# Kernel tuning notes

Measured on AMD Instinct MI355X. Metric: run time of the kernel, lower is better.

## Reference

```python
import jax, jax.numpy as jnp
import numpy as np

GRID = 5          # grid_size
DEG = 3           # spline_degree
NC = GRID + DEG   # num_coeffs = 8
IN = 4            # input_dim
HID = 4           # hidden_dim
N = 524288        # batch
TAU = 1.0         # gumbel_tau


def get_knots(knot_deltas):
    # softplus deltas normalized to span [-1, 1], then clamp-pad ends DEG times
    d = jax.nn.softplus(knot_deltas)
    dn = d / d.sum() * 2.0
    interior = -1.0 + jnp.cumsum(dn)                      # [GRID+1]
    knots = jnp.concatenate([jnp.array([-1.0], dtype=d.dtype), interior[:-1],
                             jnp.array([1.0], dtype=d.dtype)])  # [GRID+2]
    pad0 = jnp.full((DEG,), knots[0], dtype=d.dtype)
    pad1 = jnp.full((DEG,), knots[-1], dtype=d.dtype)
    return jnp.concatenate([pad0, knots, pad1])           # [GRID+2+2*DEG]


def b_spline_basis(x, knots):
    # x: [N]; Cox-de Boor recursion, degree-0 -> DEG
    xe = x[:, None]
    basis = ((xe >= knots[:-1]) & (xe < knots[1:])).astype(x.dtype)
    basis = basis.at[:, -1].add((x == knots[-1]).astype(x.dtype))
    for d in range(1, DEG + 1):
        b1, b2 = basis[:, :-1], basis[:, 1:]
        n = b1.shape[1]
        ki, kid = knots[:n], knots[d:d + n]
        ki1, kid1 = knots[1:1 + n], knots[d + 1:d + 1 + n]
        den1, den2 = kid - ki, kid1 - ki1
        m1, m2 = den1 > 1e-8, den2 > 1e-8
        t1 = jnp.where(m1, (xe - ki) / jnp.where(m1, den1, 1.0) * b1, 0.0)
        t2 = jnp.where(m2, (kid1 - xe) / jnp.where(m2, den2, 1.0) * b2, 0.0)
        basis = t1 + t2
    return basis  # [N, GRID+1+DEG] = [N, NC+1]


def spline_apply(x, coeffs, knot_deltas):
    knots = get_knots(knot_deltas)
    b = b_spline_basis(x, knots)
    if b.shape[1] > NC:
        b = b[:, :NC]
    elif b.shape[1] < NC:
        b = jnp.pad(b, ((0, 0), (0, NC - b.shape[1])))
    return b @ coeffs  # [N]


spline_v = jax.vmap(spline_apply, in_axes=(0, 0, 0))  # over edges


def setup_inputs() -> dict:
    key = jax.random.key(0)
    ks = jax.random.split(key, 8)
    x = jax.random.uniform(ks[0], (N, IN), dtype=jnp.float32, minval=-1.0, maxval=1.0)
    l1_coeffs = jax.random.normal(ks[1], (HID * IN, NC), dtype=jnp.float32)
    l1_knot_deltas = jax.random.normal(ks[2], (HID * IN, GRID + 1), dtype=jnp.float32)
    op_alpha = jax.random.normal(ks[3], (HID, 2), dtype=jnp.float32)
    u = jax.random.uniform(ks[4], (HID, 2), dtype=jnp.float32, minval=1e-6, maxval=1.0 - 1e-6)
    gumbel_noise = -jnp.log(-jnp.log(u))
    l2_coeffs = jax.random.normal(ks[5], (HID, NC), dtype=jnp.float32)
    l2_knot_deltas = jax.random.normal(ks[6], (HID, GRID + 1), dtype=jnp.float32)
    base_offset = jax.random.normal(ks[7], (1,), dtype=jnp.float32)
    return {"x": x, "l1_coeffs": l1_coeffs, "l1_knot_deltas": l1_knot_deltas,
            "op_alpha": op_alpha, "gumbel_noise": gumbel_noise,
            "l2_coeffs": l2_coeffs, "l2_knot_deltas": l2_knot_deltas,
            "base_offset": base_offset}


def reference(x, l1_coeffs, l1_knot_deltas, op_alpha, gumbel_noise,
              l2_coeffs, l2_knot_deltas, base_offset):
    xT = x.T                                              # [IN, N]
    x_edges = jnp.broadcast_to(xT[None], (HID, IN, xT.shape[1])).reshape(HID * IN, -1)
    l1 = spline_v(x_edges, l1_coeffs, l1_knot_deltas).reshape(HID, IN, -1)
    sum_v = l1.sum(axis=1)                                # [HID, N]
    prod_v = jnp.clip(l1, -5.0, 5.0).prod(axis=1)         # [HID, N]
    w = jax.nn.softmax((op_alpha + gumbel_noise) / TAU, axis=-1)  # gumbel-softmax (soft)
    hidden = w[:, 0:1] * sum_v + w[:, 1:2] * prod_v       # [HID, N]
    l2 = spline_v(hidden, l2_coeffs, l2_knot_deltas)      # [HID, N]
    return l2.sum(axis=0)[:, None] + base_offset          # [N, 1]
```

## Files before the change

### kernel.cpp

```cpp
#include <hip/hip_runtime.h>
#include <math.h>

#define GRIDK   5
#define DEG     3
#define NC      8
#define IN_DIM  4
#define HID     4
#define NKNOT   13
#define NSPL    20
#define NPTS    524288

struct SplineTabs {
    float knots[NSPL][NKNOT];
    float inv1[NSPL][12];
    float inv2[NSPL][11];
    float inv3[NSPL][10];
    float coef[NSPL][9];
    float w0[HID];
    float w1[HID];
    float base;
};

__device__ __forceinline__ float softplusf(float x) {
    return fmaxf(x, 0.0f) + log1pf(expf(-fabsf(x)));
}

__device__ __forceinline__ float spline_eval(const SplineTabs& T, int s, float x) {
    bool in_dom = (x >= -1.0f) && (x < 1.0f);
    if (!in_dom) return 0.0f;

    const float* t = T.knots[s];
    int j = 3;
    j += (x >= t[4]);
    j += (x >= t[5]);
    j += (x >= t[6]);
    j += (x >= t[7]);
    j += (x >= t[8]);

    float l1v = x - t[j];
    float l2v = x - t[j - 1];
    float l3v = x - t[j - 2];
    float r1 = t[j + 1] - x;
    float r2 = t[j + 2] - x;
    float r3 = t[j + 3] - x;

    float temp, saved;
    temp = T.inv1[s][j];
    float N0 = r1 * temp;
    float N1 = l1v * temp;
    temp = N0 * T.inv2[s][j - 1];
    N0 = r1 * temp;
    saved = l2v * temp;
    temp = N1 * T.inv2[s][j];
    N1 = saved + r2 * temp;
    float N2 = l1v * temp;
    temp = N0 * T.inv3[s][j - 2];
    N0 = r1 * temp;
    saved = l3v * temp;
    temp = N1 * T.inv3[s][j - 1];
    N1 = saved + r2 * temp;
    saved = l2v * temp;
    temp = N2 * T.inv3[s][j];
    N2 = saved + r3 * temp;
    float N3 = l1v * temp;

    const float* c = T.coef[s];
    return N0 * c[j - 3] + N1 * c[j - 2] + N2 * c[j - 1] + N3 * c[j];
}

__global__ __launch_bounds__(256) void unified_kan_kernel(
    const float* __restrict__ x,
    const float* __restrict__ l1_coeffs,
    const float* __restrict__ l1_kd,
    const float* __restrict__ op_alpha,
    const float* __restrict__ gumbel,
    const float* __restrict__ l2_coeffs,
    const float* __restrict__ l2_kd,
    const float* __restrict__ base_offset,
    float* __restrict__ out)
{
    __shared__ SplineTabs T;
    const int tid = threadIdx.x;

    if (tid < NSPL) {
        const int s = tid;
        const float* deltas;
        const float* cf;
        if (s < HID * IN_DIM) { deltas = l1_kd + s * (GRIDK + 1); cf = l1_coeffs + s * NC; }
        else                  { deltas = l2_kd + (s - HID * IN_DIM) * (GRIDK + 1);
                                cf = l2_coeffs + (s - HID * IN_DIM) * NC; }

        float d[GRIDK + 1];
        float dsum = 0.0f;
        #pragma unroll
        for (int j = 0; j < GRIDK + 1; ++j) { d[j] = softplusf(deltas[j]); dsum += d[j]; }
        float scale = 2.0f / dsum;

        float t[NKNOT];
        t[0] = t[1] = t[2] = t[3] = -1.0f;
        float acc = 0.0f;
        #pragma unroll
        for (int j = 0; j < GRIDK; ++j) { acc += d[j] * scale; t[4 + j] = -1.0f + acc; }
        t[9] = t[10] = t[11] = t[12] = 1.0f;

        #pragma unroll
        for (int i = 0; i < NKNOT; ++i) T.knots[s][i] = t[i];
        #pragma unroll
        for (int i = 0; i < 12; ++i) { float den = t[i + 1] - t[i]; T.inv1[s][i] = (den > 1e-8f) ? 1.0f / den : 0.0f; }
        #pragma unroll
        for (int i = 0; i < 11; ++i) { float den = t[i + 2] - t[i]; T.inv2[s][i] = (den > 1e-8f) ? 1.0f / den : 0.0f; }
        #pragma unroll
        for (int i = 0; i < 10; ++i) { float den = t[i + 3] - t[i]; T.inv3[s][i] = (den > 1e-8f) ? 1.0f / den : 0.0f; }
        #pragma unroll
        for (int i = 0; i < NC; ++i) T.coef[s][i] = cf[i];
        T.coef[s][8] = 0.0f;
    } else if (tid < NSPL + HID) {
        const int h = tid - NSPL;
        float a0 = op_alpha[h * 2 + 0] + gumbel[h * 2 + 0];
        float a1 = op_alpha[h * 2 + 1] + gumbel[h * 2 + 1];
        float m = fmaxf(a0, a1);
        float e0 = expf(a0 - m), e1 = expf(a1 - m);
        float inv = 1.0f / (e0 + e1);
        T.w0[h] = e0 * inv;
        T.w1[h] = e1 * inv;
    } else if (tid == NSPL + HID) {
        T.base = base_offset[0];
    }
    __syncthreads();

    const int stride = gridDim.x * blockDim.x;
    for (int i = blockIdx.x * blockDim.x + tid; i < NPTS; i += stride) {
        float4 xv = reinterpret_cast<const float4*>(x)[i];
        float xin[IN_DIM] = {xv.x, xv.y, xv.z, xv.w};

        float acc = T.base;
        #pragma unroll
        for (int h = 0; h < HID; ++h) {
            float sum = 0.0f, prod = 1.0f;
            #pragma unroll
            for (int k = 0; k < IN_DIM; ++k) {
                float v = spline_eval(T, h * IN_DIM + k, xin[k]);
                sum += v;
                prod *= fminf(fmaxf(v, -5.0f), 5.0f);
            }
            float hid = T.w0[h] * sum + T.w1[h] * prod;
            acc += spline_eval(T, HID * IN_DIM + h, hid);
        }
        out[i] = acc;
    }
}

extern "C" void kernel_launch(void* const* d_in, const int* in_sizes, int n_in,
                              void* d_out, int out_size, void* d_ws, size_t ws_size,
                              hipStream_t stream) {
    const float* x         = (const float*)d_in[0];
    const float* l1_coeffs = (const float*)d_in[1];
    const float* l1_kd     = (const float*)d_in[2];
    const float* op_alpha  = (const float*)d_in[3];
    const float* gumbel    = (const float*)d_in[4];
    const float* l2_coeffs = (const float*)d_in[5];
    const float* l2_kd     = (const float*)d_in[6];
    const float* base_off  = (const float*)d_in[7];
    float* out = (float*)d_out;

    const int block = 256;
    const int grid = 1024;
    unified_kan_kernel<<<grid, block, 0, stream>>>(
        x, l1_coeffs, l1_kd, op_alpha, gumbel, l2_coeffs, l2_kd, base_off, out);
}
```

Baseline: 96.59 us.

## Precompute per-span cubic polynomials for splines, evaluate with Horner

Each block now converts every spline's B-spline basis into per-span cubic polynomial coefficients in shared memory, with one thread per spline and span. Per-point evaluation becomes a knot-interval lookup plus one Horner evaluation instead of the Cox-de Boor recursion. The grid-stride loop is replaced by exactly two points per thread and a grid sized to cover the batch. This removes many multiplies and shared-memory table reads per spline evaluation, but moves more setup work into every block and evaluates relative to the span's left knot, which may change rounding slightly.

```diff
diff --git a/kernel.cpp b/kernel.cpp
--- a/kernel.cpp
+++ b/kernel.cpp
@@ -9,64 +9,12 @@
 #define NKNOT   13
 #define NSPL    20
 #define NPTS    524288
-
-struct SplineTabs {
-    float knots[NSPL][NKNOT];
-    float inv1[NSPL][12];
-    float inv2[NSPL][11];
-    float inv3[NSPL][10];
-    float coef[NSPL][9];
-    float w0[HID];
-    float w1[HID];
-    float base;
-};
+#define NSPAN   6
 
 __device__ __forceinline__ float softplusf(float x) {
     return fmaxf(x, 0.0f) + log1pf(expf(-fabsf(x)));
 }
 
-__device__ __forceinline__ float spline_eval(const SplineTabs& T, int s, float x) {
-    bool in_dom = (x >= -1.0f) && (x < 1.0f);
-    if (!in_dom) return 0.0f;
-
-    const float* t = T.knots[s];
-    int j = 3;
-    j += (x >= t[4]);
-    j += (x >= t[5]);
-    j += (x >= t[6]);
-    j += (x >= t[7]);
-    j += (x >= t[8]);
-
-    float l1v = x - t[j];
-    float l2v = x - t[j - 1];
-    float l3v = x - t[j - 2];
-    float r1 = t[j + 1] - x;
-    float r2 = t[j + 2] - x;
-    float r3 = t[j + 3] - x;
-
-    float temp, saved;
-    temp = T.inv1[s][j];
-    float N0 = r1 * temp;
-    float N1 = l1v * temp;
-    temp = N0 * T.inv2[s][j - 1];
-    N0 = r1 * temp;
-    saved = l2v * temp;
-    temp = N1 * T.inv2[s][j];
-    N1 = saved + r2 * temp;
-    float N2 = l1v * temp;
-    temp = N0 * T.inv3[s][j - 2];
-    N0 = r1 * temp;
-    saved = l3v * temp;
-    temp = N1 * T.inv3[s][j - 1];
-    N1 = saved + r2 * temp;
-    saved = l2v * temp;
-    temp = N2 * T.inv3[s][j];
-    N2 = saved + r3 * temp;
-    float N3 = l1v * temp;
-
-    const float* c = T.coef[s];
-    return N0 * c[j - 3] + N1 * c[j - 2] + N2 * c[j - 1] + N3 * c[j];
-}
 
 __global__ __launch_bounds__(256) void unified_kan_kernel(
     const float* __restrict__ x,
@@ -79,75 +27,170 @@
     const float* __restrict__ base_offset,
     float* __restrict__ out)
 {
-    __shared__ SplineTabs T;
+    __shared__ float4 polyS[NSPL * NSPAN];
+    __shared__ float4 kn4S[NSPL];
+    __shared__ float  kn8S[NSPL];
+    __shared__ float  w0S[HID], w1S[HID], baseS;
+
     const int tid = threadIdx.x;
 
-    if (tid < NSPL) {
-        const int s = tid;
-        const float* deltas;
-        const float* cf;
-        if (s < HID * IN_DIM) { deltas = l1_kd + s * (GRIDK + 1); cf = l1_coeffs + s * NC; }
-        else                  { deltas = l2_kd + (s - HID * IN_DIM) * (GRIDK + 1);
-                                cf = l2_coeffs + (s - HID * IN_DIM) * NC; }
+    if (tid < NSPL * NSPAN) {
+        const int s  = tid / NSPAN;
+        const int jj = 3 + (tid % NSPAN);
+
+        const float* deltas = (s < HID * IN_DIM)
+            ? l1_kd + s * (GRIDK + 1)
+            : l2_kd + (s - HID * IN_DIM) * (GRIDK + 1);
+        const float* cf = (s < HID * IN_DIM)
+            ? l1_coeffs + s * NC
+            : l2_coeffs + (s - HID * IN_DIM) * NC;
 
         float d[GRIDK + 1];
         float dsum = 0.0f;
         #pragma unroll
-        for (int j = 0; j < GRIDK + 1; ++j) { d[j] = softplusf(deltas[j]); dsum += d[j]; }
-        float scale = 2.0f / dsum;
+        for (int k = 0; k < GRIDK + 1; ++k) { d[k] = softplusf(deltas[k]); dsum += d[k]; }
+        const float scale = 2.0f / dsum;
 
         float t[NKNOT];
         t[0] = t[1] = t[2] = t[3] = -1.0f;
         float acc = 0.0f;
         #pragma unroll
-        for (int j = 0; j < GRIDK; ++j) { acc += d[j] * scale; t[4 + j] = -1.0f + acc; }
+        for (int k = 0; k < GRIDK; ++k) { acc += d[k] * scale; t[4 + k] = -1.0f + acc; }
         t[9] = t[10] = t[11] = t[12] = 1.0f;
 
-        #pragma unroll
-        for (int i = 0; i < NKNOT; ++i) T.knots[s][i] = t[i];
-        #pragma unroll
-        for (int i = 0; i < 12; ++i) { float den = t[i + 1] - t[i]; T.inv1[s][i] = (den > 1e-8f) ? 1.0f / den : 0.0f; }
-        #pragma unroll
-        for (int i = 0; i < 11; ++i) { float den = t[i + 2] - t[i]; T.inv2[s][i] = (den > 1e-8f) ? 1.0f / den : 0.0f; }
-        #pragma unroll
-        for (int i = 0; i < 10; ++i) { float den = t[i + 3] - t[i]; T.inv3[s][i] = (den > 1e-8f) ? 1.0f / den : 0.0f; }
-        #pragma unroll
-        for (int i = 0; i < NC; ++i) T.coef[s][i] = cf[i];
-        T.coef[s][8] = 0.0f;
-    } else if (tid < NSPL + HID) {
-        const int h = tid - NSPL;
+        float P[4][4];
+        #pragma unroll
+        for (int m = 0; m < 4; ++m)
+            #pragma unroll
+            for (int k = 0; k < 4; ++k) P[m][k] = 0.0f;
+        P[0][0] = 1.0f;
+
+        #pragma unroll
+        for (int dd = 1; dd <= 3; ++dd) {
+            float NP[4][4];
+            #pragma unroll
+            for (int m = 0; m < 4; ++m)
+                #pragma unroll
+                for (int k = 0; k < 4; ++k) NP[m][k] = 0.0f;
+
+            for (int m = 0; m <= dd; ++m) {
+                const int i = jj - dd + m;
+                if (m >= 1) {
+                    const float den = t[i + dd] - t[i];
+                    if (den > 1e-8f) {
+                        const float inv = 1.0f / den;
+                        const float a = (t[jj] - t[i]) * inv;
+                        #pragma unroll
+                        for (int k = 0; k < 4; ++k) NP[m][k] += a * P[m - 1][k];
+                        #pragma unroll
+                        for (int k = 1; k < 4; ++k) NP[m][k] += inv * P[m - 1][k - 1];
+                    }
+                }
+                if (m <= dd - 1) {
+                    const float den = t[i + dd + 1] - t[i + 1];
+                    if (den > 1e-8f) {
+                        const float inv = 1.0f / den;
+                        const float a = (t[i + dd + 1] - t[jj]) * inv;
+                        #pragma unroll
+                        for (int k = 0; k < 4; ++k) NP[m][k] += a * P[m][k];
+                        #pragma unroll
+                        for (int k = 1; k < 4; ++k) NP[m][k] -= inv * P[m][k - 1];
+                    }
+                }
+            }
+            #pragma unroll
+            for (int m = 0; m < 4; ++m)
+                #pragma unroll
+                for (int k = 0; k < 4; ++k) P[m][k] = NP[m][k];
+        }
+
+        float4 o = make_float4(0.f, 0.f, 0.f, 0.f);
+        #pragma unroll
+        for (int m = 0; m < 4; ++m) {
+            const int i = jj - 3 + m;
+            const float c = (i < NC) ? cf[i] : 0.0f;
+            o.x += c * P[m][0];
+            o.y += c * P[m][1];
+            o.z += c * P[m][2];
+            o.w += c * P[m][3];
+        }
+        polyS[s * NSPAN + (jj - 3)] = o;
+
+        if ((tid % NSPAN) == 0) {
+            kn4S[s] = make_float4(t[4], t[5], t[6], t[7]);
+            kn8S[s] = t[8];
+        }
+    } else if (tid < NSPL * NSPAN + HID) {
+        const int h = tid - NSPL * NSPAN;
         float a0 = op_alpha[h * 2 + 0] + gumbel[h * 2 + 0];
         float a1 = op_alpha[h * 2 + 1] + gumbel[h * 2 + 1];
         float m = fmaxf(a0, a1);
         float e0 = expf(a0 - m), e1 = expf(a1 - m);
         float inv = 1.0f / (e0 + e1);
-        T.w0[h] = e0 * inv;
-        T.w1[h] = e1 * inv;
-    } else if (tid == NSPL + HID) {
-        T.base = base_offset[0];
+        w0S[h] = e0 * inv;
+        w1S[h] = e1 * inv;
+    } else if (tid == NSPL * NSPAN + HID) {
+        baseS = base_offset[0];
     }
     __syncthreads();
 
-    const int stride = gridDim.x * blockDim.x;
-    for (int i = blockIdx.x * blockDim.x + tid; i < NPTS; i += stride) {
-        float4 xv = reinterpret_cast<const float4*>(x)[i];
-        float xin[IN_DIM] = {xv.x, xv.y, xv.z, xv.w};
-
-        float acc = T.base;
-        #pragma unroll
-        for (int h = 0; h < HID; ++h) {
-            float sum = 0.0f, prod = 1.0f;
-            #pragma unroll
-            for (int k = 0; k < IN_DIM; ++k) {
-                float v = spline_eval(T, h * IN_DIM + k, xin[k]);
-                sum += v;
-                prod *= fminf(fmaxf(v, -5.0f), 5.0f);
-            }
-            float hid = T.w0[h] * sum + T.w1[h] * prod;
-            acc += spline_eval(T, HID * IN_DIM + h, hid);
-        }
-        out[i] = acc;
+    auto eval = [&](int s, float4 kn, float k8, float xv) -> float {
+        const bool c4 = xv >= kn.x;
+        const bool c5 = xv >= kn.y;
+        const bool c6 = xv >= kn.z;
+        const bool c7 = xv >= kn.w;
+        const bool c8 = xv >= k8;
+        const int j = (int)c4 + (int)c5 + (int)c6 + (int)c7 + (int)c8;
+        float tj = -1.0f;
+        tj = c4 ? kn.x : tj;
+        tj = c5 ? kn.y : tj;
+        tj = c6 ? kn.z : tj;
+        tj = c7 ? kn.w : tj;
+        tj = c8 ? k8   : tj;
+        const float4 c = polyS[s * NSPAN + j];
+        const float u = xv - tj;
+        float v = fmaf(fmaf(fmaf(c.w, u, c.z), u, c.y), u, c.x);
+        const bool dom = (xv >= -1.0f) && (xv < 1.0f);
+        return dom ? v : 0.0f;
+    };
+
+    const int gid = blockIdx.x * blockDim.x + tid;
+    const int i0 = gid;
+    const int i1 = gid + (NPTS / 2);
+
+    const float4 xa = reinterpret_cast<const float4*>(x)[i0];
+    const float4 xb = reinterpret_cast<const float4*>(x)[i1];
+    const float x0[IN_DIM] = {xa.x, xa.y, xa.z, xa.w};
+    const float x1[IN_DIM] = {xb.x, xb.y, xb.z, xb.w};
+
+    float acc0 = baseS, acc1 = baseS;
+
+    #pragma unroll
+    for (int h = 0; h < HID; ++h) {
+        float sum0 = 0.f, sum1 = 0.f, prod0 = 1.f, prod1 = 1.f;
+        #pragma unroll
+        for (int k = 0; k < IN_DIM; ++k) {
+            const int s = h * IN_DIM + k;
+            const float4 kn = kn4S[s];
+            const float  k8 = kn8S[s];
+            const float v0 = eval(s, kn, k8, x0[k]);
+            const float v1 = eval(s, kn, k8, x1[k]);
+            sum0 += v0; sum1 += v1;
+            prod0 *= fminf(fmaxf(v0, -5.0f), 5.0f);
+            prod1 *= fminf(fmaxf(v1, -5.0f), 5.0f);
+        }
+        const float w0 = w0S[h], w1 = w1S[h];
+        const float hid0 = w0 * sum0 + w1 * prod0;
+        const float hid1 = w0 * sum1 + w1 * prod1;
+        const int s2 = HID * IN_DIM + h;
+        const float4 kn = kn4S[s2];
+        const float  k8 = kn8S[s2];
+        acc0 += eval(s2, kn, k8, hid0);
+        acc1 += eval(s2, kn, k8, hid1);
     }
+
+    out[i0] = acc0;
+    out[i1] = acc1;
 }
 
 extern "C" void kernel_launch(void* const* d_in, const int* in_sizes, int n_in,
@@ -164,7 +207,7 @@
     float* out = (float*)d_out;
 
     const int block = 256;
-    const int grid = 1024;
+    const int grid = NPTS / (block * 2);
     unified_kan_kernel<<<grid, block, 0, stream>>>(
         x, l1_coeffs, l1_kd, op_alpha, gumbel, l2_coeffs, l2_kd, base_off, out);
 }
```

Result: faster. 85.01 us (-12.0%).
